# Optimization experiments

Hardware: AMD Instinct MI355X
Metric: run time of the kernel (lower is better)

## Reference

```python
import jax, jax.numpy as jnp
import numpy as np

D_MODEL = 2048
N_HEADS = 16
HEAD_DIM = D_MODEL // N_HEADS


def setup_inputs() -> dict:
    key = jax.random.key(0)
    ks = jax.random.split(key, 5)
    s = 0.02
    return {
        "x": jax.random.normal(ks[0], (4, 2048, D_MODEL), dtype=jnp.float32),
        "w_qkv": jax.random.normal(ks[1], (D_MODEL, 3 * D_MODEL), dtype=jnp.float32) * s,
        "b_qkv": jnp.zeros((3 * D_MODEL,), dtype=jnp.float32),
        "w_out": jax.random.normal(ks[2], (D_MODEL, D_MODEL), dtype=jnp.float32) * s,
        "b_out": jnp.zeros((D_MODEL,), dtype=jnp.float32),
    }


def reference(x, w_qkv, b_qkv, w_out, b_out):
    B, T, C = x.shape
    qkv = x @ w_qkv + b_qkv  # [B,T,3C]
    q, k, v = jnp.split(qkv, 3, axis=-1)
    # [B,T,C] -> [B,H,T,hd]
    def to_heads(t):
        return t.reshape(B, T, N_HEADS, HEAD_DIM).transpose(0, 2, 1, 3)
    q, k, v = to_heads(q), to_heads(k), to_heads(v)
    scale = 1.0 / jnp.sqrt(jnp.asarray(HEAD_DIM, dtype=x.dtype))
    attn = jnp.einsum("bhqd,bhkd->bhqk", q, k) * scale
    causal = jnp.tril(jnp.ones((T, T), dtype=bool))
    attn = jnp.where(causal[None, None], attn, jnp.asarray(-jnp.inf, dtype=attn.dtype))
    attn = jax.nn.softmax(attn, axis=-1)
    out = jnp.einsum("bhqk,bhkd->bhqd", attn, v)
    out = out.transpose(0, 2, 1, 3).reshape(B, T, C)
    return out @ w_out + b_out
```

## Files before the change

kernel.cpp:

```cpp
#include <hip/hip_runtime.h>
#include <hip/hip_bf16.h>

#define DEVFN static __device__ __forceinline__

typedef __attribute__((ext_vector_type(8))) __bf16 bf16x8;
typedef __attribute__((ext_vector_type(4))) float f32x4;
typedef __attribute__((ext_vector_type(16))) float f32x16;

#define MFMA16(a, b, c) __builtin_amdgcn_mfma_f32_16x16x32_bf16(a, b, c, 0, 0, 0)
#define MFMA32(a, b, c) __builtin_amdgcn_mfma_f32_32x32x16_bf16(a, b, c, 0, 0, 0)

DEVFN void gload16(const void* g, void* l) {
  __builtin_amdgcn_global_load_lds((const __attribute__((address_space(1))) void*)g,
                                   (__attribute__((address_space(3))) void*)l, 16, 0, 0);
}

DEVFN void vwait8() { asm volatile("s_waitcnt vmcnt(8)" ::: "memory"); __builtin_amdgcn_sched_barrier(0); }
DEVFN void vwait4() { asm volatile("s_waitcnt vmcnt(4)" ::: "memory"); __builtin_amdgcn_sched_barrier(0); }
DEVFN void vwait0() { asm volatile("s_waitcnt vmcnt(0)" ::: "memory"); __builtin_amdgcn_sched_barrier(0); }
DEVFN void bar()    { __builtin_amdgcn_s_barrier(); }
DEVFN void barsched() { __builtin_amdgcn_s_barrier(); __builtin_amdgcn_sched_barrier(0); }

DEVFN unsigned pk2(float a, float b) {
  union { __bf16 h[2]; unsigned u; } z;
  z.h[0] = (__bf16)a; z.h[1] = (__bf16)b;
  return z.u;
}

DEVFN bf16x8 mk_pa(bool h1, unsigned lo0, unsigned lo1, unsigned hi0, unsigned hi1) {
  const unsigned sA = h1 ? hi0 : lo0, sB = h1 ? hi1 : lo1;
  const unsigned cA = h1 ? lo0 : hi0, cB = h1 ? lo1 : hi1;
  const unsigned rA = (unsigned)__shfl_xor((int)cA, 32);
  const unsigned rB = (unsigned)__shfl_xor((int)cB, 32);
  union { unsigned u[4]; bf16x8 v; } z;
  z.u[0] = h1 ? rA : sA; z.u[1] = h1 ? rB : sB;
  z.u[2] = h1 ? sA : rA; z.u[3] = h1 ? sB : rB;
  return z.v;
}

__global__ __launch_bounds__(256) void cvt_f32_bf16(const float* __restrict__ in,
                                                    __bf16* __restrict__ out) {
  size_t i = ((size_t)blockIdx.x * 256 + threadIdx.x) * 8;
  f32x4 a = *(const f32x4*)(in + i);
  f32x4 b = *(const f32x4*)(in + i + 4);
  bf16x8 u;
  u[0] = (__bf16)a[0]; u[1] = (__bf16)a[1]; u[2] = (__bf16)a[2]; u[3] = (__bf16)a[3];
  u[4] = (__bf16)b[0]; u[5] = (__bf16)b[1]; u[6] = (__bf16)b[2]; u[7] = (__bf16)b[3];
  *(bf16x8*)(out + i) = u;
}

__global__ __launch_bounds__(256) void transpose_w(const float* __restrict__ in,
                                                   __bf16* __restrict__ out,
                                                   int K, int N) {
  __shared__ float tile[32][33];
  const int t = threadIdx.x, tx = t & 31, ty = t >> 5;
  const int n0 = blockIdx.x * 32, k0 = blockIdx.y * 32;
#pragma unroll
  for (int r = 0; r < 4; r++)
    tile[ty + r * 8][tx] = in[(size_t)(k0 + ty + r * 8) * N + n0 + tx];
  __syncthreads();
#pragma unroll
  for (int r = 0; r < 4; r++)
    out[(size_t)(n0 + ty + r * 8) * K + k0 + tx] = (__bf16)tile[tx][ty + r * 8];
}

__global__ __launch_bounds__(256) void transpose_v(const __bf16* __restrict__ in,
                                                   __bf16* __restrict__ out) {
  __shared__ __bf16 tile[64][72];
  const int bh = blockIdx.z;
  const int t0 = blockIdx.x * 64, d0 = blockIdx.y * 64;
  const int tid = threadIdx.x;
  const int r = tid >> 3, c8 = (tid & 7) * 8;
  const __bf16* ip = in + (size_t)bh * 2048 * 128;
#pragma unroll
  for (int i = 0; i < 2; i++)
    *(bf16x8*)&tile[i * 32 + r][c8] =
        *(const bf16x8*)(ip + (size_t)(t0 + i * 32 + r) * 128 + d0 + c8);
  __syncthreads();
  __bf16* op = out + (size_t)bh * 2048 * 128;
#pragma unroll
  for (int i = 0; i < 2; i++) {
    const int dd = i * 32 + r;
    bf16x8 v;
#pragma unroll
    for (int j = 0; j < 8; j++) v[j] = tile[c8 + j][dd];
    *(bf16x8*)(op + (size_t)(d0 + dd) * 2048 + t0 + c8) = v;
  }
}

#define QK_SCALE 0.12751745f

DEVFN void stage_tile(const __bf16* gx, size_t Kst, int t, __bf16* ldst,
                      int rr, int gsw, int w) {
#pragma unroll
  for (int j = 0; j < 4; j++)
    gload16(gx + (size_t)(j * 64 + rr) * Kst + (size_t)t * 64 + gsw,
            ldst + j * 4096 + w * 512);
}

DEVFN void stage_chunk(const __bf16* gx, size_t Kst, int t, __bf16* ldst, int j,
                       int rr, int gsw, int w) {
  gload16(gx + (size_t)(j * 64 + rr) * Kst + (size_t)t * 64 + gsw,
          ldst + j * 4096 + w * 512);
}

DEVFN void tile_step(__bf16* la, __bf16* lb, f32x4 (&acc)[8][4],
                     const __bf16* ga, const __bf16* gb, size_t Kst, int t, int NT,
                     int rr, int gsw, int w, int wr, int wc, int lg, int li) {
  bf16x8 a[4][2], bl[2][2], br[2][2];
  const int sa = li & 7;
  const int arow = wr * 128 + li;
  const int brow = wc * 64 + li;
  const bool pf = (t + 2 < NT);

#pragma unroll
  for (int mi = 0; mi < 4; mi++)
#pragma unroll
    for (int ks = 0; ks < 2; ks++)
      a[mi][ks] = *(const bf16x8*)&la[(arow + mi * 16) * 64 + (((ks * 4 + lg) ^ sa) * 8)];
#pragma unroll
  for (int ni = 0; ni < 2; ni++)
#pragma unroll
    for (int ks = 0; ks < 2; ks++)
      bl[ni][ks] = *(const bf16x8*)&lb[(brow + ni * 16) * 64 + (((ks * 4 + lg) ^ sa) * 8)];
  bar();
  __builtin_amdgcn_s_setprio(1);
#pragma unroll
  for (int mi = 0; mi < 4; mi++)
#pragma unroll
    for (int ni = 0; ni < 2; ni++)
#pragma unroll
      for (int ks = 0; ks < 2; ks++)
        acc[mi][ni] = MFMA16(a[mi][ks], bl[ni][ks], acc[mi][ni]);
  __builtin_amdgcn_s_setprio(0);
  barsched();

#pragma unroll
  for (int ni = 0; ni < 2; ni++)
#pragma unroll
    for (int ks = 0; ks < 2; ks++)
      br[ni][ks] = *(const bf16x8*)&lb[(brow + (ni + 2) * 16) * 64 + (((ks * 4 + lg) ^ sa) * 8)];
  if (pf) {
    stage_chunk(ga, Kst, t + 2, la, 0, rr, gsw, w);
    stage_chunk(ga, Kst, t + 2, la, 2, rr, gsw, w);
  }
  bar();
  __builtin_amdgcn_s_setprio(1);
#pragma unroll
  for (int mi = 0; mi < 4; mi++)
#pragma unroll
    for (int ni = 0; ni < 2; ni++)
#pragma unroll
      for (int ks = 0; ks < 2; ks++)
        acc[mi][ni + 2] = MFMA16(a[mi][ks], br[ni][ks], acc[mi][ni + 2]);
  __builtin_amdgcn_s_setprio(0);
  barsched();

#pragma unroll
  for (int mi = 0; mi < 4; mi++)
#pragma unroll
    for (int ks = 0; ks < 2; ks++)
      a[mi][ks] = *(const bf16x8*)&la[(arow + (mi + 4) * 16) * 64 + (((ks * 4 + lg) ^ sa) * 8)];
  if (pf) {
    stage_chunk(gb, Kst, t + 2, lb, 0, rr, gsw, w);
    stage_chunk(gb, Kst, t + 2, lb, 1, rr, gsw, w);
  }
  bar();
  __builtin_amdgcn_s_setprio(1);
#pragma unroll
  for (int mi = 0; mi < 4; mi++)
#pragma unroll
    for (int ni = 0; ni < 2; ni++)
#pragma unroll
      for (int ks = 0; ks < 2; ks++)
        acc[mi + 4][ni] = MFMA16(a[mi][ks], bl[ni][ks], acc[mi + 4][ni]);
  __builtin_amdgcn_s_setprio(0);
  barsched();

  if (pf) {
    stage_chunk(gb, Kst, t + 2, lb, 2, rr, gsw, w);
    stage_chunk(gb, Kst, t + 2, lb, 3, rr, gsw, w);
    stage_chunk(ga, Kst, t + 2, la, 1, rr, gsw, w);
    stage_chunk(ga, Kst, t + 2, la, 3, rr, gsw, w);
  }
  __builtin_amdgcn_s_setprio(1);
#pragma unroll
  for (int mi = 0; mi < 4; mi++)
#pragma unroll
    for (int ni = 0; ni < 2; ni++)
#pragma unroll
      for (int ks = 0; ks < 2; ks++)
        acc[mi + 4][ni + 2] = MFMA16(a[mi][ks], br[ni][ks], acc[mi + 4][ni + 2]);
  __builtin_amdgcn_s_setprio(0);

  if (pf) vwait8(); else vwait0();
  bar();
}

template <int MODE>
__global__ __launch_bounds__(512, 2) void gemm256(
    const __bf16* __restrict__ A, const __bf16* __restrict__ Bt,
    const float* __restrict__ bias, int K, int Ncols,
    __bf16* __restrict__ qo, __bf16* __restrict__ ko, __bf16* __restrict__ vo,
    float* __restrict__ outf) {
  __shared__ __align__(16) __bf16 lds[65536];
  const int tid = threadIdx.x;
  const int w = tid >> 6, lane = tid & 63;
  const int wr = w >> 2, wc = w & 3;
  const int lg = lane >> 4, li = lane & 15;
  const int nbx = gridDim.x;
  const int orig = (int)blockIdx.y * nbx + (int)blockIdx.x;
  const int x = orig & 7, i = orig >> 3;
  const int xc = x & 1, xr = x >> 1;
  const int hw = nbx >> 1;
  const int band = i >> 5;
  const int j = i & 31;
  const size_t n0 = (size_t)(xc * hw + band * 4 + (j & 3)) * 256;
  const size_t m0 = (size_t)(xr * 8 + (j >> 2)) * 256;
  const int rr = tid >> 3;
  const int gsw = ((tid & 7) ^ (rr & 7)) * 8;
  const __bf16* ga = A + m0 * K;
  const __bf16* gb = Bt + n0 * K;
  const int NT = K >> 6;

  __bf16* la0 = lds;
  __bf16* la1 = lds + 16384;
  __bf16* lb0 = lds + 32768;
  __bf16* lb1 = lds + 49152;

  f32x4 acc[8][4] = {};

  stage_tile(ga, K, 0, la0, rr, gsw, w);
  stage_tile(gb, K, 0, lb0, rr, gsw, w);
  stage_tile(ga, K, 1, la1, rr, gsw, w);
  stage_tile(gb, K, 1, lb1, rr, gsw, w);
  vwait8();
  bar();

  for (int t = 0; t < NT; t += 2) {
    tile_step(la0, lb0, acc, ga, gb, K, t,     NT, rr, gsw, w, wr, wc, lg, li);
    tile_step(la1, lb1, acc, ga, gb, K, t + 1, NT, rr, gsw, w, wr, wc, lg, li);
  }

  if (MODE == 0) {
    const int which = (int)(n0 >> 11);
    const int b = (int)(m0 >> 11);
    __bf16* outp = (which == 0) ? qo : ((which == 1) ? ko : vo);
    const float scale = (which == 0) ? QK_SCALE : 1.0f;
#pragma unroll
    for (int ni = 0; ni < 4; ni++) {
      const int ncol = (int)n0 + wc * 64 + ni * 16 + li;
      const float bv = bias[ncol];
      const int h = (ncol & 2047) >> 7;
      const int d = ncol & 127;
      const size_t base = (size_t)(b * 16 + h) * (2048 * 128) + d;
#pragma unroll
      for (int mi = 0; mi < 8; mi++)
#pragma unroll
        for (int r = 0; r < 4; r++) {
          const int tt = ((int)m0 + wr * 128 + mi * 16 + lg * 4 + r) & 2047;
          outp[base + (size_t)tt * 128] = (__bf16)((acc[mi][ni][r] + bv) * scale);
        }
    }
  } else {
#pragma unroll
    for (int ni = 0; ni < 4; ni++) {
      const int ncol = (int)n0 + wc * 64 + ni * 16 + li;
      const float bv = bias[ncol];
#pragma unroll
      for (int mi = 0; mi < 8; mi++)
#pragma unroll
        for (int r = 0; r < 4; r++) {
          const size_t mrow = m0 + wr * 128 + mi * 16 + lg * 4 + r;
          outf[mrow * Ncols + ncol] = acc[mi][ni][r] + bv;
        }
    }
  }
}

DEVFN void attn_stageK(const __bf16* const (&ksrc)[4], int k0, __bf16* Kl, int w) {
#pragma unroll
  for (int i = 0; i < 4; i++)
    gload16(ksrc[i] + (size_t)k0 * 128, Kl + i * 2048 + w * 512);
}
DEVFN void attn_stageV(const __bf16* const (&vsrc)[4], int k0, __bf16* Vl, int w) {
#pragma unroll
  for (int i = 0; i < 4; i++)
    gload16(vsrc[i] + k0, Vl + i * 2048 + w * 512);
}

template <bool DIAG>
DEVFN void attn_tile(int kt, int n, int q0w, int w, int lq, int hi,
                     const __bf16* const (&ksrc)[4], const __bf16* const (&vsrc)[4],
                     __bf16* Kl, __bf16* Vl,
                     const bf16x8 (&qf)[8], f32x16 (&o)[4],
                     float& mref, float& lrow) {
  const int k0 = kt * 64;
  const bool more = (kt + 1 < n);

  vwait4();
  barsched();

  f32x16 sTa = (f32x16)(0.0f), sTb = (f32x16)(0.0f);
  const int ksw = (lq & 7) << 3;
#pragma unroll
  for (int kk = 0; kk < 8; kk++) {
    bf16x8 ka = *(const bf16x8*)&Kl[lq * 128 + ((kk * 16 + hi * 8) ^ ksw)];
    sTa = MFMA32(ka, qf[kk], sTa);
    bf16x8 kb = *(const bf16x8*)&Kl[(32 + lq) * 128 + ((kk * 16 + hi * 8) ^ ksw)];
    sTb = MFMA32(kb, qf[kk], sTb);
  }
  barsched();
  if (more) attn_stageK(ksrc, k0 + 64, Kl, w);

  float s0[16], s1[16];
#pragma unroll
  for (int r = 0; r < 16; r++) { s0[r] = sTa[r]; s1[r] = sTb[r]; }

  float vm0 = -1e30f, vm1 = -1e30f;
#pragma unroll
  for (int r = 0; r < 16; r++) {
    if (DIAG) {
      const int krow = (r & 3) + 8 * (r >> 2) + 4 * hi;
      if (k0 + krow > q0w + lq) s0[r] = -1e30f;
      if (k0 + 32 + krow > q0w + lq) s1[r] = -1e30f;
    }
    if (r & 1) vm1 = fmaxf(vm1, fmaxf(s0[r], s1[r]));
    else       vm0 = fmaxf(vm0, fmaxf(s0[r], s1[r]));
  }
  float vm = fmaxf(vm0, vm1);
  vm = fmaxf(vm, __shfl_xor(vm, 32));

  if (__any(vm - mref > 8.0f)) {
    const bool up = vm - mref > 8.0f;
    const float sc = up ? __builtin_amdgcn_exp2f(mref - vm) : 1.0f;
    if (up) mref = vm;
    lrow *= sc;
#pragma unroll
    for (int r = 0; r < 16; r++) {
      const float scr = __shfl(sc, (r & 3) + 8 * (r >> 2) + 4 * hi);
#pragma unroll
      for (int dt = 0; dt < 4; dt++) o[dt][r] *= scr;
    }
  }

  float p0 = 0.f, p1 = 0.f, p2 = 0.f, p3 = 0.f;
#pragma unroll
  for (int r = 0; r < 16; r++) {
    const float e0 = __builtin_amdgcn_exp2f(s0[r] - mref);
    const float e1 = __builtin_amdgcn_exp2f(s1[r] - mref);
    s0[r] = e0; s1[r] = e1;
    if ((r & 1) == 0) { p0 += e0; p1 += e1; } else { p2 += e0; p3 += e1; }
  }
  float ps = (p0 + p2) + (p1 + p3);
  ps += __shfl_xor(ps, 32);
  lrow += ps;

  const bool h1 = (hi != 0);
  const unsigned q00 = pk2(s0[0],  s0[1]),  q01 = pk2(s0[2],  s0[3]);
  const unsigned q02 = pk2(s0[4],  s0[5]),  q03 = pk2(s0[6],  s0[7]);
  const unsigned q04 = pk2(s0[8],  s0[9]),  q05 = pk2(s0[10], s0[11]);
  const unsigned q06 = pk2(s0[12], s0[13]), q07 = pk2(s0[14], s0[15]);
  const unsigned q10 = pk2(s1[0],  s1[1]),  q11 = pk2(s1[2],  s1[3]);
  const unsigned q12 = pk2(s1[4],  s1[5]),  q13 = pk2(s1[6],  s1[7]);
  const unsigned q14 = pk2(s1[8],  s1[9]),  q15 = pk2(s1[10], s1[11]);
  const unsigned q16 = pk2(s1[12], s1[13]), q17 = pk2(s1[14], s1[15]);
  bf16x8 pa[4];
  pa[0] = mk_pa(h1, q00, q01, q02, q03);
  pa[1] = mk_pa(h1, q04, q05, q06, q07);
  pa[2] = mk_pa(h1, q10, q11, q12, q13);
  pa[3] = mk_pa(h1, q14, q15, q16, q17);

  if (more) vwait4(); else vwait0();
  barsched();

#pragma unroll
  for (int ks = 0; ks < 4; ks++)
#pragma unroll
    for (int dt = 0; dt < 4; dt++) {
      const int d = dt * 32 + lq;
      bf16x8 vf = *(const bf16x8*)&Vl[d * 64 +
                     ((ks * 16 + hi * 8) ^ (((d ^ (d >> 3)) & 7) << 3))];
      o[dt] = MFMA32(pa[ks], vf, o[dt]);
    }
  barsched();
  if (more) attn_stageV(vsrc, k0 + 64, Vl, w);
}

DEVFN void attn_run(int qt, int bh, int w, int lq, int hi,
                    const __bf16* qp, __bf16* ob,
                    const __bf16* const (&ksrc)[4], const __bf16* const (&vsrc)[4],
                    __bf16* Kl, __bf16* Vl) {
  const int q0w = qt * 128 + w * 32;
  bf16x8 qf[8];
#pragma unroll
  for (int kk = 0; kk < 8; kk++)
    qf[kk] = *(const bf16x8*)(qp + (size_t)(q0w + lq) * 128 + kk * 16 + hi * 8);

  f32x16 o[4];
  o[0] = (f32x16)(0.0f); o[1] = (f32x16)(0.0f);
  o[2] = (f32x16)(0.0f); o[3] = (f32x16)(0.0f);
  float mref = -1e30f, lrow = 0.f;

  const int n = 2 * qt + 2;
  attn_stageK(ksrc, 0, Kl, w);
  attn_stageV(vsrc, 0, Vl, w);

  for (int kt = 0; kt < n - 2; kt++)
    attn_tile<false>(kt, n, q0w, w, lq, hi, ksrc, vsrc, Kl, Vl, qf, o, mref, lrow);
  attn_tile<true>(n - 2, n, q0w, w, lq, hi, ksrc, vsrc, Kl, Vl, qf, o, mref, lrow);
  attn_tile<true>(n - 1, n, q0w, w, lq, hi, ksrc, vsrc, Kl, Vl, qf, o, mref, lrow);

  const int b = bh >> 4, h = bh & 15;
  const float inv = 1.0f / lrow;
  float invr[16];
#pragma unroll
  for (int r = 0; r < 16; r++)
    invr[r] = __shfl(inv, (r & 3) + 8 * (r >> 2) + 4 * hi);
#pragma unroll
  for (int dt = 0; dt < 4; dt++)
#pragma unroll
    for (int r = 0; r < 16; r++) {
      const int q = q0w + (r & 3) + 8 * (r >> 2) + 4 * hi;
      ob[(size_t)(b * 2048 + q) * 2048 + h * 128 + dt * 32 + lq]
          = (__bf16)(o[dt][r] * invr[r]);
    }
}

__global__ __launch_bounds__(256, 2) void attn_fwd(
    const __bf16* __restrict__ qb, const __bf16* __restrict__ kb,
    const __bf16* __restrict__ vtb, __bf16* __restrict__ ob) {
  __shared__ __align__(16) __bf16 Kl[64 * 128];
  __shared__ __align__(16) __bf16 Vl[128 * 64];
  const int orig = (int)blockIdx.y * 8 + (int)blockIdx.x;
  const int swz = (orig & 7) * 64 + (orig >> 3);
  const int bx = swz & 7;
  const int bh = swz >> 3;
  const int tid = threadIdx.x;
  const int w = tid >> 6, l = tid & 63;
  const int lq = l & 31, hi = l >> 5;
  const int lg = l >> 4;
  const __bf16* qp = qb + (size_t)bh * (2048 * 128);
  const __bf16* kp = kb + (size_t)bh * (2048 * 128);
  const __bf16* vtp = vtb + (size_t)bh * (2048 * 128);

  const __bf16* ksrc[4];
  const __bf16* vsrc[4];
#pragma unroll
  for (int i = 0; i < 4; i++) {
    const int key = i * 16 + w * 4 + lg;
    ksrc[i] = kp + (size_t)key * 128 + 8 * ((l & 15) ^ (key & 7));
    const int d = i * 32 + (tid >> 3);
    const int g = (tid & 7) ^ ((d ^ (d >> 3)) & 7);
    vsrc[i] = vtp + (size_t)d * 2048 + g * 8;
  }

  attn_run(15 - bx, bh, w, lq, hi, qp, ob, ksrc, vsrc, Kl, Vl);
  attn_run(bx,      bh, w, lq, hi, qp, ob, ksrc, vsrc, Kl, Vl);
}

extern "C" void kernel_launch(void* const* d_in, const int* in_sizes, int n_in,
                              void* d_out, int out_size, void* d_ws, size_t ws_size,
                              hipStream_t stream) {
  (void)in_sizes; (void)n_in; (void)out_size; (void)ws_size;
  const float* x     = (const float*)d_in[0];
  const float* w_qkv = (const float*)d_in[1];
  const float* b_qkv = (const float*)d_in[2];
  const float* w_out = (const float*)d_in[3];
  const float* b_out = (const float*)d_in[4];
  float* out = (float*)d_out;
  char* ws = (char*)d_ws;

  __bf16* xb    = (__bf16*)(ws + 0);
  __bf16* wqkvT = (__bf16*)(ws + 33554432);
  __bf16* qbuf  = (__bf16*)(ws + 58720256);
  __bf16* kbuf  = (__bf16*)(ws + 92274688);
  __bf16* vbuf  = (__bf16*)(ws + 125829120);
  __bf16* woutT = (__bf16*)(ws + 159383552);

  cvt_f32_bf16<<<8192, 256, 0, stream>>>(x, xb);
  transpose_w<<<dim3(192, 64), 256, 0, stream>>>(w_qkv, wqkvT, 2048, 6144);
  transpose_w<<<dim3(64, 64), 256, 0, stream>>>(w_out, woutT, 2048, 2048);
  gemm256<0><<<dim3(24, 32), 512, 0, stream>>>(xb, wqkvT, b_qkv, 2048, 6144,
                                               qbuf, kbuf, vbuf, nullptr);
  transpose_v<<<dim3(32, 2, 64), 256, 0, stream>>>(vbuf, xb);
  attn_fwd<<<dim3(8, 64), 256, 0, stream>>>(qbuf, kbuf, xb, vbuf);
  gemm256<1><<<dim3(8, 32), 512, 0, stream>>>(vbuf, woutT, b_out, 2048, 2048,
                                              nullptr, nullptr, nullptr, out);
}
```

Measured before the change: 408.0 us.

## Fuse V transpose into QKV GEMM epilogue and simplify GEMM tile pipeline

The QKV GEMM epilogue now writes V directly in transposed [d][t] layout, so the separate transpose_v kernel and its extra round trip through memory are removed. The attention and output-projection buffers are swapped to match. The GEMM inner step is also restructured into two half-tile phases that load all four B fragments at once, stage whole tiles per phase and use fewer barriers. The transposed V stores are strided by 2048 elements and poorly coalesced, and the coarser staging may expose more load latency.

```diff
diff --git a/kernel.cpp b/kernel.cpp
--- a/kernel.cpp
+++ b/kernel.cpp
@@ -64,30 +64,6 @@
     out[(size_t)(n0 + ty + r * 8) * K + k0 + tx] = (__bf16)tile[tx][ty + r * 8];
 }
 
-__global__ __launch_bounds__(256) void transpose_v(const __bf16* __restrict__ in,
-                                                   __bf16* __restrict__ out) {
-  __shared__ __bf16 tile[64][72];
-  const int bh = blockIdx.z;
-  const int t0 = blockIdx.x * 64, d0 = blockIdx.y * 64;
-  const int tid = threadIdx.x;
-  const int r = tid >> 3, c8 = (tid & 7) * 8;
-  const __bf16* ip = in + (size_t)bh * 2048 * 128;
-#pragma unroll
-  for (int i = 0; i < 2; i++)
-    *(bf16x8*)&tile[i * 32 + r][c8] =
-        *(const bf16x8*)(ip + (size_t)(t0 + i * 32 + r) * 128 + d0 + c8);
-  __syncthreads();
-  __bf16* op = out + (size_t)bh * 2048 * 128;
-#pragma unroll
-  for (int i = 0; i < 2; i++) {
-    const int dd = i * 32 + r;
-    bf16x8 v;
-#pragma unroll
-    for (int j = 0; j < 8; j++) v[j] = tile[c8 + j][dd];
-    *(bf16x8*)(op + (size_t)(d0 + dd) * 2048 + t0 + c8) = v;
-  }
-}
-
 #define QK_SCALE 0.12751745f
 
 DEVFN void stage_tile(const __bf16* gx, size_t Kst, int t, __bf16* ldst,
@@ -98,20 +74,14 @@
             ldst + j * 4096 + w * 512);
 }
 
-DEVFN void stage_chunk(const __bf16* gx, size_t Kst, int t, __bf16* ldst, int j,
-                       int rr, int gsw, int w) {
-  gload16(gx + (size_t)(j * 64 + rr) * Kst + (size_t)t * 64 + gsw,
-          ldst + j * 4096 + w * 512);
-}
-
 DEVFN void tile_step(__bf16* la, __bf16* lb, f32x4 (&acc)[8][4],
                      const __bf16* ga, const __bf16* gb, size_t Kst, int t, int NT,
                      int rr, int gsw, int w, int wr, int wc, int lg, int li) {
-  bf16x8 a[4][2], bl[2][2], br[2][2];
   const int sa = li & 7;
   const int arow = wr * 128 + li;
   const int brow = wc * 64 + li;
   const bool pf = (t + 2 < NT);
+  bf16x8 a[4][2], b[4][2];
 
 #pragma unroll
   for (int mi = 0; mi < 4; mi++)
@@ -119,82 +89,41 @@
     for (int ks = 0; ks < 2; ks++)
       a[mi][ks] = *(const bf16x8*)&la[(arow + mi * 16) * 64 + (((ks * 4 + lg) ^ sa) * 8)];
 #pragma unroll
-  for (int ni = 0; ni < 2; ni++)
+  for (int ni = 0; ni < 4; ni++)
 #pragma unroll
     for (int ks = 0; ks < 2; ks++)
-      bl[ni][ks] = *(const bf16x8*)&lb[(brow + ni * 16) * 64 + (((ks * 4 + lg) ^ sa) * 8)];
-  bar();
+      b[ni][ks] = *(const bf16x8*)&lb[(brow + ni * 16) * 64 + (((ks * 4 + lg) ^ sa) * 8)];
   __builtin_amdgcn_s_setprio(1);
 #pragma unroll
   for (int mi = 0; mi < 4; mi++)
 #pragma unroll
-    for (int ni = 0; ni < 2; ni++)
+    for (int ni = 0; ni < 4; ni++)
 #pragma unroll
       for (int ks = 0; ks < 2; ks++)
-        acc[mi][ni] = MFMA16(a[mi][ks], bl[ni][ks], acc[mi][ni]);
+        acc[mi][ni] = MFMA16(a[mi][ks], b[ni][ks], acc[mi][ni]);
   __builtin_amdgcn_s_setprio(0);
   barsched();
-
-#pragma unroll
-  for (int ni = 0; ni < 2; ni++)
-#pragma unroll
-    for (int ks = 0; ks < 2; ks++)
-      br[ni][ks] = *(const bf16x8*)&lb[(brow + (ni + 2) * 16) * 64 + (((ks * 4 + lg) ^ sa) * 8)];
-  if (pf) {
-    stage_chunk(ga, Kst, t + 2, la, 0, rr, gsw, w);
-    stage_chunk(ga, Kst, t + 2, la, 2, rr, gsw, w);
-  }
-  bar();
-  __builtin_amdgcn_s_setprio(1);
-#pragma unroll
-  for (int mi = 0; mi < 4; mi++)
-#pragma unroll
-    for (int ni = 0; ni < 2; ni++)
-#pragma unroll
-      for (int ks = 0; ks < 2; ks++)
-        acc[mi][ni + 2] = MFMA16(a[mi][ks], br[ni][ks], acc[mi][ni + 2]);
-  __builtin_amdgcn_s_setprio(0);
-  barsched();
+  if (pf) stage_tile(gb, Kst, t + 2, lb, rr, gsw, w);
 
 #pragma unroll
   for (int mi = 0; mi < 4; mi++)
 #pragma unroll
     for (int ks = 0; ks < 2; ks++)
       a[mi][ks] = *(const bf16x8*)&la[(arow + (mi + 4) * 16) * 64 + (((ks * 4 + lg) ^ sa) * 8)];
-  if (pf) {
-    stage_chunk(gb, Kst, t + 2, lb, 0, rr, gsw, w);
-    stage_chunk(gb, Kst, t + 2, lb, 1, rr, gsw, w);
-  }
-  bar();
   __builtin_amdgcn_s_setprio(1);
 #pragma unroll
   for (int mi = 0; mi < 4; mi++)
 #pragma unroll
-    for (int ni = 0; ni < 2; ni++)
+    for (int ni = 0; ni < 4; ni++)
 #pragma unroll
       for (int ks = 0; ks < 2; ks++)
-        acc[mi + 4][ni] = MFMA16(a[mi][ks], bl[ni][ks], acc[mi + 4][ni]);
+        acc[mi + 4][ni] = MFMA16(a[mi][ks], b[ni][ks], acc[mi + 4][ni]);
   __builtin_amdgcn_s_setprio(0);
   barsched();
-
-  if (pf) {
-    stage_chunk(gb, Kst, t + 2, lb, 2, rr, gsw, w);
-    stage_chunk(gb, Kst, t + 2, lb, 3, rr, gsw, w);
-    stage_chunk(ga, Kst, t + 2, la, 1, rr, gsw, w);
-    stage_chunk(ga, Kst, t + 2, la, 3, rr, gsw, w);
-  }
-  __builtin_amdgcn_s_setprio(1);
-#pragma unroll
-  for (int mi = 0; mi < 4; mi++)
-#pragma unroll
-    for (int ni = 0; ni < 2; ni++)
-#pragma unroll
-      for (int ks = 0; ks < 2; ks++)
-        acc[mi + 4][ni + 2] = MFMA16(a[mi][ks], br[ni][ks], acc[mi + 4][ni + 2]);
-  __builtin_amdgcn_s_setprio(0);
+  if (pf) stage_tile(ga, Kst, t + 2, la, rr, gsw, w);
 
   if (pf) vwait8(); else vwait0();
-  bar();
+  barsched();
 }
 
 template <int MODE>
@@ -235,7 +164,7 @@
   stage_tile(ga, K, 1, la1, rr, gsw, w);
   stage_tile(gb, K, 1, lb1, rr, gsw, w);
   vwait8();
-  bar();
+  barsched();
 
   for (int t = 0; t < NT; t += 2) {
     tile_step(la0, lb0, acc, ga, gb, K, t,     NT, rr, gsw, w, wr, wc, lg, li);
@@ -253,13 +182,16 @@
       const float bv = bias[ncol];
       const int h = (ncol & 2047) >> 7;
       const int d = ncol & 127;
-      const size_t base = (size_t)(b * 16 + h) * (2048 * 128) + d;
+      const size_t baseN = (size_t)(b * 16 + h) * (2048 * 128) + d;
+      const size_t baseT = (size_t)(b * 16 + h) * (2048 * 128) + (size_t)d * 2048;
 #pragma unroll
       for (int mi = 0; mi < 8; mi++)
 #pragma unroll
         for (int r = 0; r < 4; r++) {
           const int tt = ((int)m0 + wr * 128 + mi * 16 + lg * 4 + r) & 2047;
-          outp[base + (size_t)tt * 128] = (__bf16)((acc[mi][ni][r] + bv) * scale);
+          const __bf16 val = (__bf16)((acc[mi][ni][r] + bv) * scale);
+          if (which == 2) outp[baseT + tt] = val;
+          else            outp[baseN + (size_t)tt * 128] = val;
         }
     }
   } else {
@@ -483,8 +415,7 @@
   transpose_w<<<dim3(64, 64), 256, 0, stream>>>(w_out, woutT, 2048, 2048);
   gemm256<0><<<dim3(24, 32), 512, 0, stream>>>(xb, wqkvT, b_qkv, 2048, 6144,
                                                qbuf, kbuf, vbuf, nullptr);
-  transpose_v<<<dim3(32, 2, 64), 256, 0, stream>>>(vbuf, xb);
-  attn_fwd<<<dim3(8, 64), 256, 0, stream>>>(qbuf, kbuf, xb, vbuf);
-  gemm256<1><<<dim3(8, 32), 512, 0, stream>>>(vbuf, woutT, b_out, 2048, 2048,
+  attn_fwd<<<dim3(8, 64), 256, 0, stream>>>(qbuf, kbuf, vbuf, xb);
+  gemm256<1><<<dim3(8, 32), 512, 0, stream>>>(xb, woutT, b_out, 2048, 2048,
                                               nullptr, nullptr, nullptr, out);
 }
```

Measured after the change: 431.8 us. +5.8%, slower.
